# Optimization experiments

Hardware: AMD Instinct MI355X
Metric: run time of the kernel (lower is better)

Reference implementation:

```python
import jax, jax.numpy as jnp
import numpy as np

B, T, D, H, C = 256, 128, 1, 2048, 10


def _xavier(key, shape):
    fan_out, fan_in = shape
    std = float(np.sqrt(2.0 / (fan_in + fan_out)))
    return jax.random.normal(key, shape, dtype=jnp.float32) * std


def setup_inputs() -> dict:
    key = jax.random.key(0)
    kx, kU, kW, kV = jax.random.split(key, 4)
    return {
        "x": jax.random.normal(kx, (B, T), dtype=jnp.float32),
        "U": _xavier(kU, (H, D)),
        "W": _xavier(kW, (H, H)),
        "V": _xavier(kV, (C, H)),
        "bh": jnp.zeros((H,), dtype=jnp.float32),
        "bp": jnp.zeros((C,), dtype=jnp.float32),
    }


def reference(x, U, W, V, bh, bp):
    # x: [B, T]; per-step input x[:, t:t+1] -> [B, 1] (input_dim == 1)
    xs = jnp.swapaxes(x, 0, 1)[:, :, None]  # [T, B, 1]

    def step(h, x_t):
        # h: [B, H]; x_t: [B, 1]
        h_new = jnp.tanh(x_t @ U.T + h @ W.T + bh)
        return h_new, None

    h0 = jnp.zeros((x.shape[0], H), dtype=x.dtype)
    h_last, _ = jax.lax.scan(step, h0, xs)
    output = h_last @ V.T + bp  # [B, C]
    return (h_last, output)
```

## Files before the change

### kernel.cpp

```cpp
#include <hip/hip_runtime.h>
#include <cmath>


#define B_ 256
#define T_ 128
#define H_ 2048
#define C_ 10

typedef _Float16 half_t;
typedef _Float16 half8 __attribute__((ext_vector_type(8)));
typedef _Float16 half4v __attribute__((ext_vector_type(4)));
typedef float floatx4 __attribute__((ext_vector_type(4)));
typedef unsigned long long u64;
typedef unsigned long long u64x2 __attribute__((ext_vector_type(2)));

#define FLAG_DWORDS (128 * 8 * 32 * 32)

__device__ __forceinline__ float fast_tanh(float v) {
    return 1.0f - 2.0f / (__expf(2.0f * v) + 1.0f);
}

__device__ __forceinline__ void publish_u64(u64* p, u64 v) {
    u64 old = __hip_atomic_exchange(p, v, __ATOMIC_RELAXED,
                                    __HIP_MEMORY_SCOPE_AGENT);
    asm volatile("" :: "v"(old));
}

__global__ void __launch_bounds__(512, 2) rnn_persist(
    const float* __restrict__ x,
    const float* __restrict__ U,
    const float* __restrict__ W,
    const float* __restrict__ bh,
    const float* __restrict__ V,
    const float* __restrict__ bp,
    half_t* __restrict__ hP0,
    half_t* __restrict__ hP1,
    float* __restrict__ hf32,
    float* __restrict__ outp,
    unsigned* __restrict__ flags)
{
    const int tid  = threadIdx.x;
    const int wave = tid >> 6, lane = tid & 63;
    const int quad = lane >> 4, lq = lane & 15;
    const int id   = blockIdx.x;
    const int g    = id & 7;
    const int C    = id >> 3;
    const int m0   = g * 32;
    const int n0   = C * 64;

    half8 Bw[8][4];
#pragma unroll
    for (int kk = 0; kk < 8; ++kk) {
#pragma unroll
        for (int nt = 0; nt < 4; ++nt) {
            const int gn = n0 + nt * 16 + lq;
            const int k0 = wave * 256 + kk * 32 + quad * 8;
            const float4 w0 = *(const float4*)&W[(size_t)gn * H_ + k0];
            const float4 w1 = *(const float4*)&W[(size_t)gn * H_ + k0 + 4];
            const float wv[8] = {w0.x, w0.y, w0.z, w0.w, w1.x, w1.y, w1.z, w1.w};
            half8 hw;
#pragma unroll
            for (int j = 0; j < 8; ++j) hw[j] = (half_t)wv[j];
            Bw[kk][nt] = hw;
        }
    }

    const int mtO = wave & 1, ntO = wave >> 1;
    const float uvO = U[n0 + ntO * 16 + lq];
    const float bvO = bh[n0 + ntO * 16 + lq];

    __shared__ floatx4 red[2][8][4][64];
    __shared__ __align__(16) float Tr[8][16][20];
    __shared__ float xs[T_][32];

    for (int i = tid; i < 32 * T_; i += 512) {
        const int r = i & 31, tt = i >> 5;
        xs[tt][r] = x[(size_t)(m0 + r) * T_ + tt];
    }
    __syncthreads();

    const int prow = (tid >> 8) * 16 + ((tid >> 1) & 15);
    const int pcol = ((tid >> 7) & 1) * 32 + ((tid >> 5) & 3) * 8 + (tid & 1) * 4;
    const size_t slab = (size_t)g * 16384;
    const size_t pdst = slab + (size_t)C * 512 + tid;
    const size_t cbase = slab + (size_t)wave * 2048 + (size_t)lane * 2;

    const int sigma = mtO * 256 + (ntO >> 1) * 128
                    + ((ntO & 1) * 2 + (quad >> 1)) * 32 + lq * 2 + (quad & 1);
    const size_t pdst_o = slab + (size_t)C * 512 + sigma;

    unsigned* myflag_base = flags + ((size_t)g * 32 + C) * 32;
    const unsigned* pollp = flags + ((size_t)g * 32 + wave * 4 + (lane & 3)) * 32;

    {
        const float xb = xs[0][prow];
        half4v hv;
#pragma unroll
        for (int j = 0; j < 4; ++j) {
            const int n = n0 + pcol + j;
            hv[j] = (half_t)fast_tanh(xb * U[n] + bh[n]);
        }
        publish_u64((u64*)hP1 + pdst, __builtin_bit_cast(u64, hv));
    }
    __syncthreads();
    if (tid == 0)
        __hip_atomic_fetch_add(myflag_base, 1u, __ATOMIC_RELAXED,
                               __HIP_MEMORY_SCOPE_AGENT);

    for (int t = 1; t < T_; ++t) {
        const half_t* hin = (t & 1) ? hP1 : hP0;
        half_t* hout      = (t & 1) ? hP0 : hP1;
        const u64* pw = (const u64*)hin + cbase;

        {
            const unsigned* fp = pollp + (size_t)(t - 1) * (8 * 32 * 32);
            while (true) {
                const unsigned v = __hip_atomic_load(fp, __ATOMIC_RELAXED,
                                                     __HIP_MEMORY_SCOPE_AGENT);
                if (__all(v >= 1u)) break;
                __builtin_amdgcn_s_sleep(1);
            }
            asm volatile("" ::: "memory");
        }

        floatx4 acc[2][4] = {};

        u64 rl[8], rh[8];
        auto issue = [&](int f) {
            const u64* q = pw + (size_t)((f >> 2) * 512 + ((f >> 1) & 1) * 256
                                         + (f & 1) * 128);
            rl[f & 7] = __hip_atomic_load(q, __ATOMIC_RELAXED,
                                          __HIP_MEMORY_SCOPE_AGENT);
            rh[f & 7] = __hip_atomic_load(q + 1, __ATOMIC_RELAXED,
                                          __HIP_MEMORY_SCOPE_AGENT);
        };
#pragma unroll
        for (int f = 0; f < 8; ++f) issue(f);
#pragma unroll
        for (int f = 0; f < 16; ++f) {
            const int cp = f >> 2, mt = (f >> 1) & 1, kc = f & 1;
            const int kk = cp * 2 + kc;
            u64x2 bits; bits.x = rl[f & 7]; bits.y = rh[f & 7];
            const half8 av = __builtin_bit_cast(half8, bits);
            if (f + 8 < 16) issue(f + 8);
            acc[mt][0] = __builtin_amdgcn_mfma_f32_16x16x32_f16(av, Bw[kk][0], acc[mt][0], 0, 0, 0);
            acc[mt][1] = __builtin_amdgcn_mfma_f32_16x16x32_f16(av, Bw[kk][1], acc[mt][1], 0, 0, 0);
            acc[mt][2] = __builtin_amdgcn_mfma_f32_16x16x32_f16(av, Bw[kk][2], acc[mt][2], 0, 0, 0);
            acc[mt][3] = __builtin_amdgcn_mfma_f32_16x16x32_f16(av, Bw[kk][3], acc[mt][3], 0, 0, 0);
        }

#pragma unroll
        for (int mt = 0; mt < 2; ++mt)
#pragma unroll
            for (int nt = 0; nt < 4; ++nt)
                red[mt][wave][nt][lane] = acc[mt][nt];
        __syncthreads();

        {
            float xr[4];
#pragma unroll
            for (int r = 0; r < 4; ++r) xr[r] = xs[t][mtO * 16 + quad * 4 + r];
            floatx4 s = red[mtO][0][ntO][lane];
#pragma unroll
            for (int ww = 1; ww < 8; ++ww) s += red[mtO][ww][ntO][lane];
#pragma unroll
            for (int r = 0; r < 4; ++r) {
                const float pre = s[r] + xr[r] * uvO + bvO;
                Tr[wave][quad * 4 + r][lq] = fast_tanh(pre);
            }
            const float4 fr = *(const float4*)&Tr[wave][lq][quad * 4];

            if (t < T_ - 1) {
                half4v hv;
                hv[0] = (half_t)fr.x; hv[1] = (half_t)fr.y;
                hv[2] = (half_t)fr.z; hv[3] = (half_t)fr.w;
                publish_u64((u64*)hout + pdst_o, __builtin_bit_cast(u64, hv));
                __syncthreads();
                if (tid == 0)
                    __hip_atomic_fetch_add(
                        myflag_base + (size_t)t * (8 * 32 * 32), 1u,
                        __ATOMIC_RELAXED, __HIP_MEMORY_SCOPE_AGENT);
            } else {
                float* fd = hf32 + (size_t)(m0 + mtO * 16 + lq) * H_
                          + n0 + ntO * 16 + quad * 4;
                *(float4*)fd = make_float4(fr.x, fr.y, fr.z, fr.w);
                __syncthreads();
                if (tid < 32 * C_) {
                    const int r = tid & 31, c = tid >> 5;
                    float sacc = (C == 0) ? bp[c] : 0.0f;
                    const float* vr = V + (size_t)c * H_ + n0;
#pragma unroll 8
                    for (int n = 0; n < 64; ++n)
                        sacc += Tr[(n >> 4) * 2 + (r >> 4)][r & 15][n & 15] * vr[n];
                    atomicAdd(&outp[(size_t)(m0 + r) * C_ + c], sacc);
                }
            }
        }
    }
}

extern "C" void kernel_launch(void* const* d_in, const int* in_sizes, int n_in,
                              void* d_out, int out_size, void* d_ws, size_t ws_size,
                              hipStream_t stream) {
    const float* x  = (const float*)d_in[0];
    const float* U  = (const float*)d_in[1];
    const float* W  = (const float*)d_in[2];
    const float* V  = (const float*)d_in[3];
    const float* bh = (const float*)d_in[4];
    const float* bp = (const float*)d_in[5];

    float* out_h = (float*)d_out;
    float* outp  = out_h + (size_t)B_ * H_;

    half_t* hP0 = (half_t*)d_ws;
    half_t* hP1 = hP0 + (size_t)B_ * H_;
    unsigned* flags = (unsigned*)((char*)d_ws + 2u * 1024 * 1024);

    hipMemsetAsync(flags, 0, FLAG_DWORDS * sizeof(unsigned), stream);
    hipMemsetAsync(outp, 0, (size_t)B_ * C_ * sizeof(float), stream);

    rnn_persist<<<dim3(256), dim3(512), 0, stream>>>(
        x, U, W, bh, V, bp, hP0, hP1, out_h, outp, flags);
}
```

Measured before the change: 650.0 us.

## Use per-timestep rotating hidden-state buffers to allow plain vector loads

Gives every timestep its own hidden-state buffer in the workspace (127 slots) when the workspace is large enough, instead of ping-ponging between two. With no buffer ever reused, reads of the previous state can be ordinary 128-bit vector loads rather than pairs of relaxed 64-bit atomic loads, which should cut load instruction count and latency on the critical path. Plain loads may be served from stale cache lines, but fresh addresses make that unlikely. The fallback path keeps the double-buffer scheme if the workspace is too small, and the change uses far more workspace memory.

```diff
diff --git a/kernel.cpp b/kernel.cpp
--- a/kernel.cpp
+++ b/kernel.cpp
@@ -14,6 +14,9 @@
 typedef unsigned long long u64;
 typedef unsigned long long u64x2 __attribute__((ext_vector_type(2)));
 
+#define BUF_U64 131072
+#define NSLOT 127
+
 #define FLAG_DWORDS (128 * 8 * 32 * 32)
 
 __device__ __forceinline__ float fast_tanh(float v) {
@@ -26,6 +29,13 @@
     asm volatile("" :: "v"(old));
 }
 
+template <int ROT>
+__device__ __forceinline__ size_t slot_base(int s) {
+    return ROT ? (size_t)s * BUF_U64
+               : (size_t)((s + 1) & 1) * BUF_U64;
+}
+
+template <int ROT>
 __global__ void __launch_bounds__(512, 2) rnn_persist(
     const float* __restrict__ x,
     const float* __restrict__ U,
@@ -33,8 +43,7 @@
     const float* __restrict__ bh,
     const float* __restrict__ V,
     const float* __restrict__ bp,
-    half_t* __restrict__ hP0,
-    half_t* __restrict__ hP1,
+    half_t* __restrict__ hbase,
     float* __restrict__ hf32,
     float* __restrict__ outp,
     unsigned* __restrict__ flags)
@@ -100,7 +109,8 @@
             const int n = n0 + pcol + j;
             hv[j] = (half_t)fast_tanh(xb * U[n] + bh[n]);
         }
-        publish_u64((u64*)hP1 + pdst, __builtin_bit_cast(u64, hv));
+        publish_u64((u64*)hbase + slot_base<ROT>(0) + pdst,
+                    __builtin_bit_cast(u64, hv));
     }
     __syncthreads();
     if (tid == 0)
@@ -108,9 +118,8 @@
                                __HIP_MEMORY_SCOPE_AGENT);
 
     for (int t = 1; t < T_; ++t) {
-        const half_t* hin = (t & 1) ? hP1 : hP0;
-        half_t* hout      = (t & 1) ? hP0 : hP1;
-        const u64* pw = (const u64*)hin + cbase;
+        const u64* pw = (const u64*)hbase + slot_base<ROT>(t - 1) + cbase;
+        u64* pout     = (u64*)hbase + slot_base<ROT>(t);
 
         {
             const unsigned* fp = pollp + (size_t)(t - 1) * (8 * 32 * 32);
@@ -129,10 +138,16 @@
         auto issue = [&](int f) {
             const u64* q = pw + (size_t)((f >> 2) * 512 + ((f >> 1) & 1) * 256
                                          + (f & 1) * 128);
-            rl[f & 7] = __hip_atomic_load(q, __ATOMIC_RELAXED,
-                                          __HIP_MEMORY_SCOPE_AGENT);
-            rh[f & 7] = __hip_atomic_load(q + 1, __ATOMIC_RELAXED,
-                                          __HIP_MEMORY_SCOPE_AGENT);
+            if (ROT) {
+                const u64x2 v = *(const u64x2*)q;
+                rl[f & 7] = v.x;
+                rh[f & 7] = v.y;
+            } else {
+                rl[f & 7] = __hip_atomic_load(q, __ATOMIC_RELAXED,
+                                              __HIP_MEMORY_SCOPE_AGENT);
+                rh[f & 7] = __hip_atomic_load(q + 1, __ATOMIC_RELAXED,
+                                              __HIP_MEMORY_SCOPE_AGENT);
+            }
         };
 #pragma unroll
         for (int f = 0; f < 8; ++f) issue(f);
@@ -174,7 +189,7 @@
                 half4v hv;
                 hv[0] = (half_t)fr.x; hv[1] = (half_t)fr.y;
                 hv[2] = (half_t)fr.z; hv[3] = (half_t)fr.w;
-                publish_u64((u64*)hout + pdst_o, __builtin_bit_cast(u64, hv));
+                publish_u64(pout + pdst_o, __builtin_bit_cast(u64, hv));
                 __syncthreads();
                 if (tid == 0)
                     __hip_atomic_fetch_add(
@@ -212,13 +227,19 @@
     float* out_h = (float*)d_out;
     float* outp  = out_h + (size_t)B_ * H_;
 
-    half_t* hP0 = (half_t*)d_ws;
-    half_t* hP1 = hP0 + (size_t)B_ * H_;
-    unsigned* flags = (unsigned*)((char*)d_ws + 2u * 1024 * 1024);
+    unsigned* flags = (unsigned*)d_ws;
+    half_t* hbase = (half_t*)((char*)d_ws + (size_t)4 * 1024 * 1024);
+
+    const size_t need = (size_t)(4 + NSLOT) * 1024 * 1024;
+    const int rot = ws_size >= need;
 
     hipMemsetAsync(flags, 0, FLAG_DWORDS * sizeof(unsigned), stream);
     hipMemsetAsync(outp, 0, (size_t)B_ * C_ * sizeof(float), stream);
 
-    rnn_persist<<<dim3(256), dim3(512), 0, stream>>>(
-        x, U, W, bh, V, bp, hP0, hP1, out_h, outp, flags);
-}
+    if (rot)
+        rnn_persist<1><<<dim3(256), dim3(512), 0, stream>>>(
+            x, U, W, bh, V, bp, hbase, out_h, outp, flags);
+    else
+        rnn_persist<0><<<dim3(256), dim3(512), 0, stream>>>(
+            x, U, W, bh, V, bp, hbase, out_h, outp, flags);
+}
```

New measurement: 587.1 us. -9.7%, faster.
